# Kernel optimization log

Hardware: AMD Instinct MI355X
Metric: run time of the kernel (lower is better)

The kernel has to match this reference:

```python
import jax, jax.numpy as jnp
import numpy as np

B, S, CTXD, QD, ATTD = 32, 4096, 512, 512, 256

def setup_inputs() -> dict:
    key = jax.random.key(0)
    ks = jax.random.split(key, 7)
    qry = jax.random.normal(ks[0], (B, QD), dtype=jnp.float32)
    ctx = jax.random.normal(ks[1], (B, S, CTXD), dtype=jnp.float32)
    ctx_mask = jax.random.randint(ks[2], (B, S), 0, 2, dtype=jnp.int32)
    # ensure no all-zero row (would make softmax NaN)
    ctx_mask = ctx_mask.at[:, 0].set(1)
    sc = 1.0 / np.sqrt(CTXD + QD)
    W = jax.random.uniform(ks[3], (CTXD + QD, ATTD), jnp.float32, -sc, sc)
    b = jax.random.uniform(ks[4], (ATTD,), jnp.float32, -sc, sc)
    sc2 = 1.0 / np.sqrt(ATTD)
    w2 = jax.random.uniform(ks[5], (ATTD, 1), jnp.float32, -sc2, sc2)
    b2 = jax.random.uniform(ks[6], (1,), jnp.float32, -sc2, sc2)
    return {"qry": qry, "ctx": ctx, "ctx_mask": ctx_mask, "W": W, "b": b, "w2": w2, "b2": b2}

def reference(qry, ctx, ctx_mask, W, b, w2, b2):
    # cat([ctx, qry_rep]) @ W == ctx @ W_ctx + qry @ W_qry ; avoids the [B,S,ctxdim+qdim] concat
    W_ctx, W_qry = W[:CTXD], W[CTXD:]
    h = jnp.einsum('bsc,ca->bsa', ctx, W_ctx) + (qry @ W_qry)[:, None, :] + b  # [B,S,ATTD]
    y = jnp.tanh(h)
    scores = jnp.einsum('bsa,a->bs', y, w2[:, 0]) + b2[0]  # [B,S]
    scores = scores + jnp.log(ctx_mask.astype(jnp.float32))
    alphas = jax.nn.softmax(scores, axis=-1)  # [B,S]
    summary = jnp.einsum('bsc,bs->bc', ctx, alphas)  # [B,CTXD]
    return (alphas, summary, scores)
```

## Files before the change

kernel.cpp:

```cpp
#include <hip/hip_runtime.h>
#include <math.h>

#define B_ 32
#define S_ 4096
#define CTXD_ 512
#define QD_ 512
#define ATTD_ 256

#define KT 32
#define RT 64

#define MASKED_SCORE (-1e30f)

typedef __attribute__((ext_vector_type(8))) short bf16x8;
typedef __attribute__((ext_vector_type(4))) float f32x4;

__device__ __forceinline__ unsigned short f2bf(float f) {
    unsigned u = __float_as_uint(f);
    u += 0x7fff + ((u >> 16) & 1);
    return (unsigned short)(u >> 16);
}
__device__ __forceinline__ unsigned pk2(float lo, float hi) {
    return (unsigned)f2bf(lo) | ((unsigned)f2bf(hi) << 16);
}

__device__ __forceinline__ float fast_tanh(float x) {
    float xc = fminf(fmaxf(x, -15.f), 15.f);
    float t = __expf(2.f * xc);
    return (t - 1.f) / (t + 1.f);
}

__global__ __launch_bounds__(256) void wt_kernel(const float* __restrict__ W,
                                                 unsigned short* __restrict__ Wt) {
    const int n = blockIdx.x;
    const int t = threadIdx.x;
    Wt[n * CTXD_ + t] = f2bf(W[(size_t)t * ATTD_ + n]);
    Wt[n * CTXD_ + t + 256] = f2bf(W[(size_t)(t + 256) * ATTD_ + n]);
}

__global__ __launch_bounds__(256) void qh_kernel(const float* __restrict__ qry,
                                                 const float* __restrict__ W,
                                                 const float* __restrict__ bias,
                                                 float* __restrict__ qh) {
    __shared__ float q[QD_];
    const int b = blockIdx.x, t = threadIdx.x;
    for (int i = t; i < QD_; i += 256) q[i] = qry[b * QD_ + i];
    __syncthreads();
    float acc = bias[t];
    const float* Wq = W + (size_t)CTXD_ * ATTD_ + t;
    #pragma unroll 8
    for (int k = 0; k < QD_; ++k) acc += q[k] * Wq[(size_t)k * ATTD_];
    qh[b * ATTD_ + t] = acc;
}

__global__ __launch_bounds__(256, 3) void scores_kernel(
    const float* __restrict__ ctx, const unsigned short* __restrict__ Wt,
    const float* __restrict__ qh, const float* __restrict__ w2,
    const float* __restrict__ b2, const int* __restrict__ mask,
    float* __restrict__ scores) {
    __shared__ unsigned char lds_a[RT * 80];
    __shared__ unsigned char lds_b[ATTD_ * 80];
    const int t = threadIdx.x;
    const int b = blockIdx.y;
    const int s0 = blockIdx.x * RT;
    const int tx = t & 63;
    const int w = t >> 6;

    f32x4 c0, c1, c2, c3, c4, c5, c6, c7, c8, c9, c10, c11, c12, c13, c14, c15;
    c0 = c1 = c2 = c3 = c4 = c5 = c6 = c7 = (f32x4)0.f;
    c8 = c9 = c10 = c11 = c12 = c13 = c14 = c15 = (f32x4)0.f;

    const float* ctxb = ctx + ((size_t)b * S_ + s0) * CTXD_;
    const int arow = t >> 2;
    const int akq = t & 3;
    const int bn0 = (t >> 2);
    const int bn1 = bn0 + 64, bn2 = bn0 + 128, bn3 = bn0 + 192;

    const unsigned char* a_rd =
        lds_a + (w * 16 + (tx & 15)) * 80 + (tx >> 4) * 16;
    const int frow = tx & 15;
    const int fko = (tx >> 4) * 16;

    const float* sA = ctxb + (size_t)arow * CTXD_ + akq * 8;
    float4 pa0 = ((const float4*)sA)[0];
    float4 pa1 = ((const float4*)sA)[1];
    uint4 pb0 = *(const uint4*)(Wt + (size_t)bn0 * CTXD_ + akq * 8);
    uint4 pb1 = *(const uint4*)(Wt + (size_t)bn1 * CTXD_ + akq * 8);
    uint4 pb2 = *(const uint4*)(Wt + (size_t)bn2 * CTXD_ + akq * 8);
    uint4 pb3 = *(const uint4*)(Wt + (size_t)bn3 * CTXD_ + akq * 8);

    #pragma unroll 1
    for (int k0 = 0; k0 < CTXD_; k0 += KT) {
        __syncthreads();
        {
            uint4 p;
            p.x = pk2(pa0.x, pa0.y); p.y = pk2(pa0.z, pa0.w);
            p.z = pk2(pa1.x, pa1.y); p.w = pk2(pa1.z, pa1.w);
            *(uint4*)(lds_a + arow * 80 + akq * 16) = p;
            *(uint4*)(lds_b + bn0 * 80 + akq * 16) = pb0;
            *(uint4*)(lds_b + bn1 * 80 + akq * 16) = pb1;
            *(uint4*)(lds_b + bn2 * 80 + akq * 16) = pb2;
            *(uint4*)(lds_b + bn3 * 80 + akq * 16) = pb3;
        }
        __syncthreads();
        if (k0 + KT < CTXD_) {
            const float* sA2 = ctxb + (size_t)arow * CTXD_ + (k0 + KT) + akq * 8;
            pa0 = ((const float4*)sA2)[0];
            pa1 = ((const float4*)sA2)[1];
            const int kb = k0 + KT + akq * 8;
            pb0 = *(const uint4*)(Wt + (size_t)bn0 * CTXD_ + kb);
            pb1 = *(const uint4*)(Wt + (size_t)bn1 * CTXD_ + kb);
            pb2 = *(const uint4*)(Wt + (size_t)bn2 * CTXD_ + kb);
            pb3 = *(const uint4*)(Wt + (size_t)bn3 * CTXD_ + kb);
        }

        bf16x8 af = *(const bf16x8*)a_rd;
#define MFMA_T(C, NT)                                                        \
    {                                                                        \
        bf16x8 bf = *(const bf16x8*)(lds_b + ((NT)*16 + frow) * 80 + fko);   \
        C = __builtin_amdgcn_mfma_f32_16x16x32_bf16(af, bf, C, 0, 0, 0);     \
    }
        MFMA_T(c0, 0)  MFMA_T(c1, 1)  MFMA_T(c2, 2)  MFMA_T(c3, 3)
        MFMA_T(c4, 4)  MFMA_T(c5, 5)  MFMA_T(c6, 6)  MFMA_T(c7, 7)
        MFMA_T(c8, 8)  MFMA_T(c9, 9)  MFMA_T(c10, 10) MFMA_T(c11, 11)
        MFMA_T(c12, 12) MFMA_T(c13, 13) MFMA_T(c14, 14) MFMA_T(c15, 15)
#undef MFMA_T
    }

    const float* qhb = qh + b * ATTD_;
    float p0 = 0.f, p1 = 0.f, p2 = 0.f, p3 = 0.f;
#define EPI(C, NT)                                                           \
    {                                                                        \
        float qv = qhb[(NT)*16 + frow];                                      \
        float wv = w2[(NT)*16 + frow];                                       \
        p0 += fast_tanh(C[0] + qv) * wv;                                     \
        p1 += fast_tanh(C[1] + qv) * wv;                                     \
        p2 += fast_tanh(C[2] + qv) * wv;                                     \
        p3 += fast_tanh(C[3] + qv) * wv;                                     \
    }
    EPI(c0, 0)  EPI(c1, 1)  EPI(c2, 2)  EPI(c3, 3)
    EPI(c4, 4)  EPI(c5, 5)  EPI(c6, 6)  EPI(c7, 7)
    EPI(c8, 8)  EPI(c9, 9)  EPI(c10, 10) EPI(c11, 11)
    EPI(c12, 12) EPI(c13, 13) EPI(c14, 14) EPI(c15, 15)
#undef EPI
    #pragma unroll
    for (int off = 1; off <= 8; off <<= 1) {
        p0 += __shfl_xor(p0, off, 64);
        p1 += __shfl_xor(p1, off, 64);
        p2 += __shfl_xor(p2, off, 64);
        p3 += __shfl_xor(p3, off, 64);
    }
    if (frow == 0) {
        const int rbase = s0 + w * 16 + (tx >> 4) * 4;
        const float b2v = b2[0];
        float pr[4] = {p0, p1, p2, p3};
        #pragma unroll
        for (int r = 0; r < 4; ++r) {
            int s = rbase + r;
            float sc = pr[r] + b2v;
            if (mask[b * S_ + s] == 0) sc = MASKED_SCORE;
            scores[b * S_ + s] = sc;
        }
    }
}

__global__ __launch_bounds__(256) void softmax_kernel(
    const float* __restrict__ scores, float* __restrict__ alphas) {
    const int b = blockIdx.x, t = threadIdx.x;
    __shared__ float red[256];
    float v[16];
    float m = -INFINITY;
    #pragma unroll
    for (int i = 0; i < 16; ++i) {
        v[i] = scores[b * S_ + t + i * 256];
        m = fmaxf(m, v[i]);
    }
    red[t] = m;
    __syncthreads();
    for (int o = 128; o >= 1; o >>= 1) {
        if (t < o) red[t] = fmaxf(red[t], red[t + o]);
        __syncthreads();
    }
    m = red[0];
    __syncthreads();
    float sum = 0.f;
    #pragma unroll
    for (int i = 0; i < 16; ++i) {
        v[i] = expf(v[i] - m);
        sum += v[i];
    }
    red[t] = sum;
    __syncthreads();
    for (int o = 128; o >= 1; o >>= 1) {
        if (t < o) red[t] += red[t + o];
        __syncthreads();
    }
    float inv = 1.0f / red[0];
    #pragma unroll
    for (int i = 0; i < 16; ++i)
        alphas[b * S_ + t + i * 256] = v[i] * inv;
}

__global__ __launch_bounds__(256) void summary_part_kernel(
    const float* __restrict__ ctx, const float* __restrict__ alphas,
    float* __restrict__ part, int nch, int cs) {
    const int b = blockIdx.y, ch = blockIdx.x, t = threadIdx.x;
    const int col4 = t & 127;
    const int half = t >> 7;
    const int s0 = ch * cs;
    float4 acc = make_float4(0.f, 0.f, 0.f, 0.f);
    const float* cp = ctx + ((size_t)b * S_ + s0) * CTXD_;
    #pragma unroll 2
    for (int s = half; s < cs; s += 2) {
        float al = alphas[b * S_ + s0 + s];
        float4 v = ((const float4*)(cp + (size_t)s * CTXD_))[col4];
        acc.x += v.x * al; acc.y += v.y * al;
        acc.z += v.z * al; acc.w += v.w * al;
    }
    __shared__ float4 buf[128];
    if (half == 1) buf[col4] = acc;
    __syncthreads();
    if (half == 0) {
        float4 o = buf[col4];
        acc.x += o.x; acc.y += o.y; acc.z += o.z; acc.w += o.w;
        ((float4*)(part + ((size_t)(b * nch + ch)) * CTXD_))[col4] = acc;
    }
}

__global__ __launch_bounds__(256) void summary_reduce_kernel(
    const float* __restrict__ part, float* __restrict__ summary, int nch) {
    const int b = blockIdx.x, t = threadIdx.x;
    for (int c = t; c < CTXD_; c += 256) {
        float s = 0.f;
        for (int ch = 0; ch < nch; ++ch)
            s += part[((size_t)(b * nch + ch)) * CTXD_ + c];
        summary[b * CTXD_ + c] = s;
    }
}

extern "C" void kernel_launch(void* const* d_in, const int* in_sizes, int n_in,
                              void* d_out, int out_size, void* d_ws,
                              size_t ws_size, hipStream_t stream) {
    const float* qry = (const float*)d_in[0];
    const float* ctx = (const float*)d_in[1];
    const int* mask = (const int*)d_in[2];
    const float* W = (const float*)d_in[3];
    const float* bias = (const float*)d_in[4];
    const float* w2 = (const float*)d_in[5];
    const float* b2 = (const float*)d_in[6];

    float* out = (float*)d_out;
    float* alphas = out;
    float* summary = out + B_ * S_;
    float* scores = out + B_ * S_ + B_ * CTXD_;

    unsigned short* Wt = (unsigned short*)d_ws;
    float* qh = (float*)((char*)d_ws + (size_t)ATTD_ * CTXD_ * 2);
    float* part = qh + B_ * ATTD_;
    const size_t fixed_bytes = (size_t)ATTD_ * CTXD_ * 2 + (size_t)B_ * ATTD_ * 4;

    int nch = 64;
    while (nch > 1 && fixed_bytes + (size_t)B_ * nch * CTXD_ * 4 > ws_size)
        nch >>= 1;
    const int cs = S_ / nch;

    wt_kernel<<<ATTD_, 256, 0, stream>>>(W, Wt);
    qh_kernel<<<B_, 256, 0, stream>>>(qry, W, bias, qh);
    scores_kernel<<<dim3(S_ / RT, B_), 256, 0, stream>>>(ctx, Wt, qh, w2, b2,
                                                         mask, scores);
    softmax_kernel<<<B_, 256, 0, stream>>>(scores, alphas);
    summary_part_kernel<<<dim3(nch, B_), 256, 0, stream>>>(ctx, alphas, part,
                                                           nch, cs);
    summary_reduce_kernel<<<B_, 256, 0, stream>>>(part, summary, nch);
}
```

Baseline: 508.5 us.

## Use 2x2 wave tiling with KT=64 in scores GEMM; widen summary partial loop

```diff
diff --git a/kernel.cpp b/kernel.cpp
--- a/kernel.cpp
+++ b/kernel.cpp
@@ -7,7 +7,7 @@
 #define QD_ 512
 #define ATTD_ 256
 
-#define KT 32
+#define KT 64
 #define RT 64
 
 #define MASKED_SCORE (-1e30f)
@@ -58,109 +58,133 @@
     const float* __restrict__ qh, const float* __restrict__ w2,
     const float* __restrict__ b2, const int* __restrict__ mask,
     float* __restrict__ scores) {
-    __shared__ unsigned char lds_a[RT * 80];
-    __shared__ unsigned char lds_b[ATTD_ * 80];
+    __shared__ unsigned char lds_a[RT * 144];
+    __shared__ unsigned char lds_b[ATTD_ * 144];
     const int t = threadIdx.x;
     const int b = blockIdx.y;
     const int s0 = blockIdx.x * RT;
     const int tx = t & 63;
     const int w = t >> 6;
-
-    f32x4 c0, c1, c2, c3, c4, c5, c6, c7, c8, c9, c10, c11, c12, c13, c14, c15;
-    c0 = c1 = c2 = c3 = c4 = c5 = c6 = c7 = (f32x4)0.f;
-    c8 = c9 = c10 = c11 = c12 = c13 = c14 = c15 = (f32x4)0.f;
+    const int wm = w & 1;
+    const int wn = w >> 1;
+    const int frow = tx & 15;
+    const int fq = tx >> 4;
+
+    f32x4 c00, c01, c02, c03, c04, c05, c06, c07;
+    f32x4 c10, c11, c12, c13, c14, c15, c16, c17;
+    c00 = c01 = c02 = c03 = c04 = c05 = c06 = c07 = (f32x4)0.f;
+    c10 = c11 = c12 = c13 = c14 = c15 = c16 = c17 = (f32x4)0.f;
 
     const float* ctxb = ctx + ((size_t)b * S_ + s0) * CTXD_;
     const int arow = t >> 2;
     const int akq = t & 3;
-    const int bn0 = (t >> 2);
-    const int bn1 = bn0 + 64, bn2 = bn0 + 128, bn3 = bn0 + 192;
-
-    const unsigned char* a_rd =
-        lds_a + (w * 16 + (tx & 15)) * 80 + (tx >> 4) * 16;
-    const int frow = tx & 15;
-    const int fko = (tx >> 4) * 16;
-
-    const float* sA = ctxb + (size_t)arow * CTXD_ + akq * 8;
-    float4 pa0 = ((const float4*)sA)[0];
-    float4 pa1 = ((const float4*)sA)[1];
-    uint4 pb0 = *(const uint4*)(Wt + (size_t)bn0 * CTXD_ + akq * 8);
-    uint4 pb1 = *(const uint4*)(Wt + (size_t)bn1 * CTXD_ + akq * 8);
-    uint4 pb2 = *(const uint4*)(Wt + (size_t)bn2 * CTXD_ + akq * 8);
-    uint4 pb3 = *(const uint4*)(Wt + (size_t)bn3 * CTXD_ + akq * 8);
+    const int bn = t;
+
+    const unsigned char* aBase = lds_a + (wm * 32 + frow) * 144 + fq * 16;
+    const unsigned char* bBase = lds_b + (wn * 128 + frow) * 144 + fq * 16;
+
+    const float* sA = ctxb + (size_t)arow * CTXD_ + akq * 16;
+    float4 fa0 = ((const float4*)sA)[0];
+    float4 fa1 = ((const float4*)sA)[1];
+    float4 fa2 = ((const float4*)sA)[2];
+    float4 fa3 = ((const float4*)sA)[3];
+    const uint4* sB = (const uint4*)(Wt + (size_t)bn * CTXD_);
+    uint4 pb0 = sB[0], pb1 = sB[1], pb2 = sB[2], pb3 = sB[3];
+    uint4 pb4 = sB[4], pb5 = sB[5], pb6 = sB[6], pb7 = sB[7];
+
+#define MM1(ni, ks, C0, C1)                                                  \
+    {                                                                        \
+        bf16x8 bf = *(const bf16x8*)(bBase + (ni) * (16 * 144) + (ks) * 64); \
+        C0 = __builtin_amdgcn_mfma_f32_16x16x32_bf16(a0, bf, C0, 0, 0, 0);   \
+        C1 = __builtin_amdgcn_mfma_f32_16x16x32_bf16(a1, bf, C1, 0, 0, 0);   \
+    }
+#define MMK(ks)                                                              \
+    {                                                                        \
+        bf16x8 a0 = *(const bf16x8*)(aBase + (ks) * 64);                     \
+        bf16x8 a1 = *(const bf16x8*)(aBase + 16 * 144 + (ks) * 64);          \
+        MM1(0, ks, c00, c10) MM1(1, ks, c01, c11) MM1(2, ks, c02, c12)       \
+        MM1(3, ks, c03, c13) MM1(4, ks, c04, c14) MM1(5, ks, c05, c15)       \
+        MM1(6, ks, c06, c16) MM1(7, ks, c07, c17)                            \
+    }
 
     #pragma unroll 1
     for (int k0 = 0; k0 < CTXD_; k0 += KT) {
         __syncthreads();
         {
             uint4 p;
-            p.x = pk2(pa0.x, pa0.y); p.y = pk2(pa0.z, pa0.w);
-            p.z = pk2(pa1.x, pa1.y); p.w = pk2(pa1.z, pa1.w);
-            *(uint4*)(lds_a + arow * 80 + akq * 16) = p;
-            *(uint4*)(lds_b + bn0 * 80 + akq * 16) = pb0;
-            *(uint4*)(lds_b + bn1 * 80 + akq * 16) = pb1;
-            *(uint4*)(lds_b + bn2 * 80 + akq * 16) = pb2;
-            *(uint4*)(lds_b + bn3 * 80 + akq * 16) = pb3;
+            p.x = pk2(fa0.x, fa0.y); p.y = pk2(fa0.z, fa0.w);
+            p.z = pk2(fa1.x, fa1.y); p.w = pk2(fa1.z, fa1.w);
+            *(uint4*)(lds_a + arow * 144 + akq * 32) = p;
+            p.x = pk2(fa2.x, fa2.y); p.y = pk2(fa2.z, fa2.w);
+            p.z = pk2(fa3.x, fa3.y); p.w = pk2(fa3.z, fa3.w);
+            *(uint4*)(lds_a + arow * 144 + akq * 32 + 16) = p;
+            uint4* bw = (uint4*)(lds_b + bn * 144);
+            bw[0] = pb0; bw[1] = pb1; bw[2] = pb2; bw[3] = pb3;
+            bw[4] = pb4; bw[5] = pb5; bw[6] = pb6; bw[7] = pb7;
         }
         __syncthreads();
         if (k0 + KT < CTXD_) {
-            const float* sA2 = ctxb + (size_t)arow * CTXD_ + (k0 + KT) + akq * 8;
-            pa0 = ((const float4*)sA2)[0];
-            pa1 = ((const float4*)sA2)[1];
-            const int kb = k0 + KT + akq * 8;
-            pb0 = *(const uint4*)(Wt + (size_t)bn0 * CTXD_ + kb);
-            pb1 = *(const uint4*)(Wt + (size_t)bn1 * CTXD_ + kb);
-            pb2 = *(const uint4*)(Wt + (size_t)bn2 * CTXD_ + kb);
-            pb3 = *(const uint4*)(Wt + (size_t)bn3 * CTXD_ + kb);
+            const float* sA2 = ctxb + (size_t)arow * CTXD_ + (k0 + KT) + akq * 16;
+            fa0 = ((const float4*)sA2)[0];
+            fa1 = ((const float4*)sA2)[1];
+            fa2 = ((const float4*)sA2)[2];
+            fa3 = ((const float4*)sA2)[3];
+            const uint4* sB2 = (const uint4*)(Wt + (size_t)bn * CTXD_ + (k0 + KT));
+            pb0 = sB2[0]; pb1 = sB2[1]; pb2 = sB2[2]; pb3 = sB2[3];
+            pb4 = sB2[4]; pb5 = sB2[5]; pb6 = sB2[6]; pb7 = sB2[7];
         }
-
-        bf16x8 af = *(const bf16x8*)a_rd;
-#define MFMA_T(C, NT)                                                        \
+        MMK(0)
+        MMK(1)
+    }
+#undef MMK
+#undef MM1
+
+    const float* qhb = qh + b * ATTD_ + wn * 128;
+    const float* w2b = w2 + wn * 128;
+    float p00 = 0.f, p01 = 0.f, p02 = 0.f, p03 = 0.f;
+    float p10 = 0.f, p11 = 0.f, p12 = 0.f, p13 = 0.f;
+#define EPI(ni, C0, C1)                                                      \
     {                                                                        \
-        bf16x8 bf = *(const bf16x8*)(lds_b + ((NT)*16 + frow) * 80 + fko);   \
-        C = __builtin_amdgcn_mfma_f32_16x16x32_bf16(af, bf, C, 0, 0, 0);     \
-    }
-        MFMA_T(c0, 0)  MFMA_T(c1, 1)  MFMA_T(c2, 2)  MFMA_T(c3, 3)
-        MFMA_T(c4, 4)  MFMA_T(c5, 5)  MFMA_T(c6, 6)  MFMA_T(c7, 7)
-        MFMA_T(c8, 8)  MFMA_T(c9, 9)  MFMA_T(c10, 10) MFMA_T(c11, 11)
-        MFMA_T(c12, 12) MFMA_T(c13, 13) MFMA_T(c14, 14) MFMA_T(c15, 15)
-#undef MFMA_T
-    }
-
-    const float* qhb = qh + b * ATTD_;
-    float p0 = 0.f, p1 = 0.f, p2 = 0.f, p3 = 0.f;
-#define EPI(C, NT)                                                           \
-    {                                                                        \
-        float qv = qhb[(NT)*16 + frow];                                      \
-        float wv = w2[(NT)*16 + frow];                                       \
-        p0 += fast_tanh(C[0] + qv) * wv;                                     \
-        p1 += fast_tanh(C[1] + qv) * wv;                                     \
-        p2 += fast_tanh(C[2] + qv) * wv;                                     \
-        p3 += fast_tanh(C[3] + qv) * wv;                                     \
-    }
-    EPI(c0, 0)  EPI(c1, 1)  EPI(c2, 2)  EPI(c3, 3)
-    EPI(c4, 4)  EPI(c5, 5)  EPI(c6, 6)  EPI(c7, 7)
-    EPI(c8, 8)  EPI(c9, 9)  EPI(c10, 10) EPI(c11, 11)
-    EPI(c12, 12) EPI(c13, 13) EPI(c14, 14) EPI(c15, 15)
+        float qv = qhb[(ni) * 16 + frow];                                    \
+        float wv = w2b[(ni) * 16 + frow];                                    \
+        p00 += fast_tanh(C0[0] + qv) * wv;                                   \
+        p01 += fast_tanh(C0[1] + qv) * wv;                                   \
+        p02 += fast_tanh(C0[2] + qv) * wv;                                   \
+        p03 += fast_tanh(C0[3] + qv) * wv;                                   \
+        p10 += fast_tanh(C1[0] + qv) * wv;                                   \
+        p11 += fast_tanh(C1[1] + qv) * wv;                                   \
+        p12 += fast_tanh(C1[2] + qv) * wv;                                   \
+        p13 += fast_tanh(C1[3] + qv) * wv;                                   \
+    }
+    EPI(0, c00, c10) EPI(1, c01, c11) EPI(2, c02, c12) EPI(3, c03, c13)
+    EPI(4, c04, c14) EPI(5, c05, c15) EPI(6, c06, c16) EPI(7, c07, c17)
 #undef EPI
     #pragma unroll
     for (int off = 1; off <= 8; off <<= 1) {
-        p0 += __shfl_xor(p0, off, 64);
-        p1 += __shfl_xor(p1, off, 64);
-        p2 += __shfl_xor(p2, off, 64);
-        p3 += __shfl_xor(p3, off, 64);
-    }
+        p00 += __shfl_xor(p00, off, 64);
+        p01 += __shfl_xor(p01, off, 64);
+        p02 += __shfl_xor(p02, off, 64);
+        p03 += __shfl_xor(p03, off, 64);
+        p10 += __shfl_xor(p10, off, 64);
+        p11 += __shfl_xor(p11, off, 64);
+        p12 += __shfl_xor(p12, off, 64);
+        p13 += __shfl_xor(p13, off, 64);
+    }
+    float* sred = (float*)lds_a;
+    __syncthreads();
     if (frow == 0) {
-        const int rbase = s0 + w * 16 + (tx >> 4) * 4;
-        const float b2v = b2[0];
-        float pr[4] = {p0, p1, p2, p3};
-        #pragma unroll
-        for (int r = 0; r < 4; ++r) {
-            int s = rbase + r;
-            float sc = pr[r] + b2v;
-            if (mask[b * S_ + s] == 0) sc = MASKED_SCORE;
-            scores[b * S_ + s] = sc;
-        }
+        const int base = wn * 64 + wm * 32 + fq * 4;
+        sred[base + 0] = p00; sred[base + 1] = p01;
+        sred[base + 2] = p02; sred[base + 3] = p03;
+        sred[base + 16 + 0] = p10; sred[base + 16 + 1] = p11;
+        sred[base + 16 + 2] = p12; sred[base + 16 + 3] = p13;
+    }
+    __syncthreads();
+    if (t < 64) {
+        const int s = s0 + t;
+        float sc = sred[t] + sred[64 + t] + b2[0];
+        if (mask[b * S_ + s] == 0) sc = MASKED_SCORE;
+        scores[b * S_ + s] = sc;
     }
 }
 
@@ -205,25 +229,36 @@
     const float* __restrict__ ctx, const float* __restrict__ alphas,
     float* __restrict__ part, int nch, int cs) {
     const int b = blockIdx.y, ch = blockIdx.x, t = threadIdx.x;
-    const int col4 = t & 127;
-    const int half = t >> 7;
+    const int col = t & 63;
+    const int q = t >> 6;
     const int s0 = ch * cs;
-    float4 acc = make_float4(0.f, 0.f, 0.f, 0.f);
+    float4 alo = make_float4(0.f, 0.f, 0.f, 0.f);
+    float4 ahi = make_float4(0.f, 0.f, 0.f, 0.f);
     const float* cp = ctx + ((size_t)b * S_ + s0) * CTXD_;
-    #pragma unroll 2
-    for (int s = half; s < cs; s += 2) {
-        float al = alphas[b * S_ + s0 + s];
-        float4 v = ((const float4*)(cp + (size_t)s * CTXD_))[col4];
-        acc.x += v.x * al; acc.y += v.y * al;
-        acc.z += v.z * al; acc.w += v.w * al;
-    }
-    __shared__ float4 buf[128];
-    if (half == 1) buf[col4] = acc;
-    __syncthreads();
-    if (half == 0) {
-        float4 o = buf[col4];
-        acc.x += o.x; acc.y += o.y; acc.z += o.z; acc.w += o.w;
-        ((float4*)(part + ((size_t)(b * nch + ch)) * CTXD_))[col4] = acc;
+    const float* ap = alphas + b * S_ + s0;
+    #pragma unroll 4
+    for (int s = q; s < cs; s += 4) {
+        float al = ap[s];
+        const float4* row = (const float4*)(cp + (size_t)s * CTXD_);
+        float4 v0 = row[col];
+        float4 v1 = row[col + 64];
+        alo.x += v0.x * al; alo.y += v0.y * al;
+        alo.z += v0.z * al; alo.w += v0.w * al;
+        ahi.x += v1.x * al; ahi.y += v1.y * al;
+        ahi.z += v1.z * al; ahi.w += v1.w * al;
+    }
+    __shared__ float4 buf[4][128];
+    buf[q][col] = alo;
+    buf[q][col + 64] = ahi;
+    __syncthreads();
+    if (t < 128) {
+        float4 a0 = buf[0][t], a1 = buf[1][t], a2 = buf[2][t], a3 = buf[3][t];
+        float4 r;
+        r.x = a0.x + a1.x + a2.x + a3.x;
+        r.y = a0.y + a1.y + a2.y + a3.y;
+        r.z = a0.z + a1.z + a2.z + a3.z;
+        r.w = a0.w + a1.w + a2.w + a3.w;
+        ((float4*)(part + ((size_t)(b * nch + ch)) * CTXD_))[t] = r;
     }
 }
 
```

Measured after the change: 519.5 us. 1.02x slower.
